# Kernel optimization log

Hardware: AMD Instinct MI355X
Metric: run time of the kernel (lower is better)

## Reference

```python
import jax, jax.numpy as jnp
import numpy as np

LRELU = 0.01  # torch nn.LeakyReLU default slope

def _lrelu(x):
    return jnp.where(x >= 0, x, LRELU * x)

def setup_inputs() -> dict:
    key = jax.random.key(0)
    ks = jax.random.split(key, 10)
    B, Cin, Cout, H, W, K, FD, LAT = 16, 256, 256, 64, 64, 3, 128, 128
    y = jax.random.normal(ks[0], (B, Cin, H, W), jnp.float32)
    finger = jax.random.randint(ks[1], (B, FD), 0, 2).astype(jnp.float32)
    ori_weight = jax.random.normal(ks[2], (Cout, Cin, K, K), jnp.float32) * 0.05
    w_mask = jax.random.normal(ks[3], (Cout, Cin, 1, 1), jnp.float32)
    f_weight = ori_weight[None]  # param initialized as 1*ori_weight, shape [1,Cout,Cin,K,K]
    style_w1 = jax.random.normal(ks[4], (LAT, FD), jnp.float32) / np.sqrt(FD)
    style_w2 = jax.random.normal(ks[5], (2 * Cin * K * K, LAT), jnp.float32) / np.sqrt(LAT)
    ori_bias = jax.random.normal(ks[6], (Cout,), jnp.float32) * 0.05
    b_mask = jax.random.normal(ks[7], (Cout,), jnp.float32)
    f_bias = ori_bias[None]  # [1,Cout]
    bias_w1 = jax.random.normal(ks[8], (Cout, FD), jnp.float32) / np.sqrt(FD)
    bias_w2 = jax.random.normal(ks[9], (Cout, Cout), jnp.float32) / np.sqrt(Cout)
    return dict(y=y, finger=finger, ori_weight=ori_weight, w_mask=w_mask,
                f_weight=f_weight, style_w1=style_w1, style_w2=style_w2,
                ori_bias=ori_bias, b_mask=b_mask, f_bias=f_bias,
                bias_w1=bias_w1, bias_w2=bias_w2)

def reference(y, finger, ori_weight, w_mask, f_weight, style_w1, style_w2,
              ori_bias, b_mask, f_bias, bias_w1, bias_w2):
    B = y.shape[0]
    Cout, Cin, K, _ = ori_weight.shape
    relu6 = lambda v: jnp.clip(v, 0.0, 6.0)
    # mask blending coefficients (w_mask broadcasts over the KxK taps, as in .repeat)
    f_w_weight = (6.0 - relu6(w_mask)) / 6.0          # [Cout,Cin,1,1]
    f_w_bias = (6.0 - relu6(b_mask)) / 6.0            # [Cout]
    mean_ori = ori_weight.mean()
    std_ori = jnp.std(ori_weight, ddof=1)             # torch .std() is unbiased
    # ApplyStyle: finger -> LAT -> 2*Cin*K*K scale/shift applied to f_weight
    h = _lrelu(finger @ style_w1.T)                   # [B,LAT]
    style = (h @ style_w2.T).reshape(B, 2, 1, Cin, K, K)
    s_weight = f_weight * (style[:, 0] + 1.0) + style[:, 1]  # [B,Cout,Cin,K,K]
    fw = f_w_weight[None]
    w1 = (1.0 - fw) * ori_weight[None] + fw * s_weight
    # per-sample whole-tensor re-standardization to ori stats
    mean = w1.mean(axis=(1, 2, 3, 4), keepdims=True)
    std = jnp.std(w1, axis=(1, 2, 3, 4), keepdims=True, ddof=1)
    w2 = (w1 - mean) / std * std_ori + mean_ori
    new_weight = (1.0 - fw) * ori_weight[None] + fw * w2      # [B,Cout,Cin,K,K]
    # per-sample bias
    s_bias = f_bias * _lrelu(_lrelu(finger @ bias_w1.T) @ bias_w2.T)  # [B,Cout]
    new_bias = (1.0 - f_w_bias) * ori_bias + f_w_bias * s_bias        # [B,Cout]
    pad = K // 2
    def conv_one(xi, wi, bi):
        o = jax.lax.conv_general_dilated(xi[None], wi, (1, 1),
                                         [(pad, pad), (pad, pad)],
                                         dimension_numbers=('NCHW', 'OIHW', 'NCHW'))
        return o[0] + bi[:, None, None]
    return jax.vmap(conv_one)(y, new_weight, new_bias)   # [B,Cout,H,W]
```

## Files before the change

kernel.cpp:

```cpp
#include <hip/hip_runtime.h>
#include <math.h>

#define LSLOPE 0.01f

__device__ __forceinline__ float lrelu(float x){ return x >= 0.f ? x : LSLOPE * x; }

typedef __attribute__((ext_vector_type(8))) short short8;
typedef __attribute__((ext_vector_type(4))) float f32x4;

__device__ __forceinline__ unsigned short f2bf(float f){
  union { float f; unsigned u; } v; v.f = f;
  unsigned r = v.u + 0x7FFFu + ((v.u >> 16) & 1u);
  return (unsigned short)(r >> 16);
}

__device__ __forceinline__ void gload_lds16(const unsigned short* g, unsigned short* l){
  __builtin_amdgcn_global_load_lds((const __attribute__((address_space(1))) unsigned int*)(g),
                                   (__attribute__((address_space(3))) unsigned int*)(l), 16, 0, 0);
}

constexpr int B    = 16;
constexpr int CIN  = 256;
constexpr int COUT = 256;
constexpr int HH   = 64;
constexpr int WW   = 64;
constexpr int FD   = 128;
constexpr int LAT  = 128;
constexpr int WPS  = CIN * 9;
constexpr int WTOT = COUT * WPS;
constexpr int HP   = 66;

constexpr int OFF_STAT  = 0;
constexpr int OFF_BMEAN = 16;
constexpr int OFF_BSTD  = 32;
constexpr int OFF_C     = 64;
constexpr int OFF_STYLE = OFF_C + 11 * WPS;
constexpr int OFF_NBIAS = OFF_STYLE + B * 2 * WPS;
constexpr int OFF_NW    = OFF_NBIAS + B * COUT;
constexpr int OFF_YTR   = OFF_NW + (B * 9 * COUT * CIN) / 2;

constexpr int PADT = 264;
constexpr int NB_CF = 9;
constexpr int NB_SB = B * 18 + B;
constexpr int NB_YT = HP * B;

__global__ __launch_bounds__(256) void k_prep1(const float* __restrict__ y, unsigned short* __restrict__ ytrp,
                                               const float* __restrict__ ow, const float* __restrict__ fwgt,
                                               const float* __restrict__ wmask, float* __restrict__ C,
                                               const float* __restrict__ finger, const float* __restrict__ sw1,
                                               const float* __restrict__ sw2, float* __restrict__ style,
                                               const float* __restrict__ bw1, const float* __restrict__ bw2,
                                               const float* __restrict__ fbias, const float* __restrict__ bmask,
                                               const float* __restrict__ obias, float* __restrict__ nbias){
  __shared__ __align__(16) char shraw[64 * PADT * 2];
  const int blk = blockIdx.x;
  const int tid = threadIdx.x;

  if (blk < NB_CF){
    const int rem = blk * 256 + tid;
    const int ic = rem / 9;
    float a_ow = 0.f, q_ow = 0.f, ab = 0.f, qb = 0.f;
    float a1 = 0.f, a2 = 0.f, d1 = 0.f, d2 = 0.f, d3 = 0.f, d4 = 0.f, d5 = 0.f;
    for (int oc = 0; oc < COUT; ++oc){
      float w = ow[(size_t)oc * WPS + rem];
      float f = fwgt[(size_t)oc * WPS + rem];
      float m = wmask[oc * CIN + ic];
      float fw = (6.f - fminf(fmaxf(m, 0.f), 6.f)) * (1.f / 6.f);
      float base = w + fw * (f - w);
      float c1 = fw * f, c2 = fw;
      a_ow += w; q_ow += w * w;
      ab += base; qb += base * base;
      a1 += c1; a2 += c2;
      d1 += c1 * c1; d2 += c2 * c2; d3 += base * c1; d4 += base * c2; d5 += c1 * c2;
    }
    C[(size_t)0  * WPS + rem] = a_ow; C[(size_t)1  * WPS + rem] = q_ow;
    C[(size_t)2  * WPS + rem] = ab;   C[(size_t)3  * WPS + rem] = qb;
    C[(size_t)4  * WPS + rem] = a1;   C[(size_t)5  * WPS + rem] = a2;
    C[(size_t)6  * WPS + rem] = d1;   C[(size_t)7  * WPS + rem] = d2;
    C[(size_t)8  * WPS + rem] = d3;   C[(size_t)9  * WPS + rem] = d4;
    C[(size_t)10 * WPS + rem] = d5;
  } else if (blk < NB_CF + NB_SB){
    float* sh = (float*)shraw;
    const int blk2 = blk - NB_CF;
    if (blk2 < B * 18){
      const int b = blk2 / 18, j0 = (blk2 - b * 18) * 256;
      if (tid < LAT){
        float a = 0.f;
        const float* fg = finger + b * FD;
        const float* w = sw1 + (size_t)tid * FD;
        for (int f = 0; f < FD; ++f) a += fg[f] * w[f];
        sh[tid] = lrelu(a);
      }
      __syncthreads();
      const int j = j0 + tid;
      float a = 0.f;
      const float* w2 = sw2 + (size_t)j * LAT;
      for (int l = 0; l < LAT; ++l) a += sh[l] * w2[l];
      style[(size_t)b * 2 * WPS + j] = a;
    } else {
      const int b = blk2 - B * 18, o = tid;
      float acc = 0.f;
      for (int f = 0; f < FD; ++f) acc += finger[b * FD + f] * bw1[o * FD + f];
      sh[o] = lrelu(acc);
      __syncthreads();
      float t = 0.f;
      for (int c = 0; c < COUT; ++c) t += sh[c] * bw2[o * COUT + c];
      t = lrelu(t);
      float sb = fbias[o] * t;
      float fwb = (6.f - fminf(fmaxf(bmask[o], 0.f), 6.f)) * (1.f / 6.f);
      nbias[b * COUT + o] = (1.f - fwb) * obias[o] + fwb * sb;
    }
  } else {
    unsigned short* t = (unsigned short*)shraw;
    const int blk3 = blk - NB_CF - NB_SB;
    const int ghp = blk3 % HP, b = blk3 / HP;
    unsigned short* dst = ytrp + ((size_t)b * HP + ghp) * HP * CIN;
    if (ghp == 0 || ghp == HP - 1){
      for (int c = tid; c < HP * CIN / 8; c += 256) ((uint4*)dst)[c] = (uint4){0, 0, 0, 0};
      return;
    }
    const int h = ghp - 1;
    const float* src = y + (size_t)b * CIN * HH * WW + h * WW;
    #pragma unroll
    for (int k = 0; k < 16; ++k){
      int idx = tid + k * 256;
      int ic = idx >> 4, w4 = (idx & 15) * 4;
      float4 v = *(const float4*)(src + (size_t)ic * HH * WW + w4);
      t[(w4 + 0) * PADT + ic] = f2bf(v.x);
      t[(w4 + 1) * PADT + ic] = f2bf(v.y);
      t[(w4 + 2) * PADT + ic] = f2bf(v.z);
      t[(w4 + 3) * PADT + ic] = f2bf(v.w);
    }
    __syncthreads();
    for (int c = tid; c < HP * CIN / 8; c += 256){
      int gwp = c >> 5, icg = (c & 31) * 8;
      uint4 v = (uint4){0, 0, 0, 0};
      if (gwp >= 1 && gwp <= 64) v = *(const uint4*)(&t[(gwp - 1) * PADT + icg]);
      ((uint4*)dst)[c] = v;
    }
  }
}

__global__ __launch_bounds__(256) void k_wstats(const float* __restrict__ C, const float* __restrict__ style,
                                                float* stat, float* bmean, float* bstd){
  __shared__ float rs[4][4];
  const int b = blockIdx.x, tid = threadIdx.x;
  const int lane = tid & 63, wid = tid >> 6;
  const float* st = style + (size_t)b * 2 * WPS;
  float s = 0.f, q = 0.f, so = 0.f, qo = 0.f;
  for (int k = 0; k < 9; ++k){
    int rem = k * 256 + tid;
    float aow = C[0 * WPS + rem], qow = C[1 * WPS + rem];
    float ab  = C[2 * WPS + rem], qb  = C[3 * WPS + rem];
    float a1  = C[4 * WPS + rem], a2  = C[5 * WPS + rem];
    float d1  = C[6 * WPS + rem], d2  = C[7 * WPS + rem];
    float d3  = C[8 * WPS + rem], d4  = C[9 * WPS + rem], d5 = C[10 * WPS + rem];
    float s0 = st[rem], s1 = st[WPS + rem];
    so += aow; qo += qow;
    s += ab + s0 * a1 + s1 * a2;
    q += qb + s0 * s0 * d1 + s1 * s1 * d2 + 2.f * (s0 * d3 + s1 * d4 + s0 * s1 * d5);
  }
  for (int o = 32; o > 0; o >>= 1){
    s += __shfl_down(s, o); q += __shfl_down(q, o);
    so += __shfl_down(so, o); qo += __shfl_down(qo, o);
  }
  if (lane == 0){ rs[0][wid] = s; rs[1][wid] = q; rs[2][wid] = so; rs[3][wid] = qo; }
  __syncthreads();
  if (tid == 0){
    const float N = (float)WTOT;
    float S = rs[0][0] + rs[0][1] + rs[0][2] + rs[0][3];
    float Q = rs[1][0] + rs[1][1] + rs[1][2] + rs[1][3];
    bmean[b] = S / N;
    bstd[b]  = sqrtf((Q - S * S / N) / (N - 1.f));
    if (b == 0){
      float SO = rs[2][0] + rs[2][1] + rs[2][2] + rs[2][3];
      float QO = rs[3][0] + rs[3][1] + rs[3][2] + rs[3][3];
      stat[0] = SO / N;
      stat[1] = sqrtf((QO - SO * SO / N) / (N - 1.f));
    }
  }
}

__global__ __launch_bounds__(256) void k_new_weight4(const float* __restrict__ ow, const float* __restrict__ fwgt,
                                                     const float* __restrict__ wmask, const float* __restrict__ style,
                                                     const float* __restrict__ stat, const float* __restrict__ bmean,
                                                     const float* __restrict__ bstd, unsigned short* __restrict__ nw){
  __shared__ float ows[WPS];
  __shared__ float fws[WPS];
  __shared__ float sts[2 * WPS];
  const int bi = blockIdx.x, oc = blockIdx.y;
  const int tid = threadIdx.x;
  const float mean_ori = stat[0], std_ori = stat[1];
  const float* owr = ow + (size_t)oc * WPS;
  const float* fwr = fwgt + (size_t)oc * WPS;
  for (int i = tid; i < WPS; i += 256){ ows[i] = owr[i]; fws[i] = fwr[i]; }
  const float fw = (6.f - fminf(fmaxf(wmask[oc * CIN + tid], 0.f), 6.f)) * (1.f / 6.f);
  #pragma unroll
  for (int bb = 0; bb < 2; ++bb){
    const int b = bi * 2 + bb;
    __syncthreads();
    const float* st = style + (size_t)b * 2 * WPS;
    for (int i = tid; i < 2 * WPS; i += 256) sts[i] = st[i];
    __syncthreads();
    const float bm = bmean[b], bs = bstd[b];
    #pragma unroll
    for (int t = 0; t < 9; ++t){
      int rem = tid * 9 + t;
      float owv = ows[rem];
      float sw = fws[rem] * (sts[rem] + 1.f) + sts[WPS + rem];
      float w1 = owv + fw * (sw - owv);
      float w2 = (w1 - bm) / bs * std_ori + mean_ori;
      nw[((size_t)(b * 9 + t) * COUT + oc) * CIN + tid] = f2bf(owv + fw * (w2 - owv));
    }
  }
}

__global__ __launch_bounds__(256, 2) void k_conv_mfma11(const unsigned short* __restrict__ ytrp,
                                                        const unsigned short* __restrict__ nw,
                                                        const float* __restrict__ nbias,
                                                        float* __restrict__ out){
  __shared__ __align__(16) unsigned short Wa[3 * 128 * 32];
  __shared__ __align__(16) unsigned short Yt[288 * 32];
  __shared__ float bsh[128];

  const int bid = blockIdx.x;
  const int xcd = bid & 7;
  const int b   = ((bid >> 8) << 3) | xcd;
  const int oc0 = ((bid >> 3) & 1) * 128;
  const int hwt = (bid >> 4) & 15;
  const int tid = threadIdx.x;
  const int lane = tid & 63, wid = tid >> 6;
  const int wr = wid >> 1, wc = wid & 1;
  const int hw0 = hwt * 256;
  const int h0  = hwt * 4;

  if (tid < 128) bsh[tid] = nbias[b * COUT + oc0 + tid];

  f32x4 acc[4][8];
  #pragma unroll
  for (int i = 0; i < 4; ++i)
    #pragma unroll
    for (int j = 0; j < 8; ++j) acc[i][j] = (f32x4){0.f, 0.f, 0.f, 0.f};

  const unsigned short* nwb = nw + ((size_t)(b * 9) * COUT + oc0) * CIN;
  const unsigned short* ytb = ytrp + (size_t)b * HP * HP * CIN;

  int a_tap[6], a_go[6], a_lo[6];
  #pragma unroll
  for (int s = 0; s < 6; ++s){
    int I = wid + 4 * s;
    int tap = I >> 3, rowbase = (I & 7) * 16;
    int row = rowbase + (lane >> 2), p = lane & 3;
    int g = p ^ ((row >> 1) & 3);
    a_tap[s] = tap;
    a_go[s]  = row * CIN + g * 8;
    a_lo[s]  = (tap * 128 + rowbase) * 32;
  }
  int y_go[5], y_lo[5]; bool y_has[5];
  #pragma unroll
  for (int s = 0; s < 5; ++s){
    int I = wid + 4 * s;
    y_has[s] = (I < 18);
    int Ic = y_has[s] ? I : 0;
    int site = Ic * 16 + (lane >> 2);
    int srow = site / 72;
    int scol = site - srow * 72;
    int gwp  = scol > 65 ? 65 : scol;
    int p = lane & 3, g = p ^ ((site >> 1) & 3);
    y_go[s] = ((h0 + srow + 1) * HP + gwp) * CIN + g * 8;
    y_lo[s] = Ic * 16 * 32;
  }

  const int gq = lane >> 4;
  int a_rb[4];
  #pragma unroll
  for (int mi = 0; mi < 4; ++mi){
    int r = wr * 64 + mi * 16 + (lane & 15);
    a_rb[mi] = r * 64 + ((gq ^ ((r >> 1) & 3)) << 4);
  }
  int b_site[8];
  #pragma unroll
  for (int ni = 0; ni < 8; ++ni)
    b_site[ni] = (wc * 2 + (ni >> 2)) * 72 + (ni & 3) * 16 + (lane & 15);

  #define STAGE(IT)                                                                 \
    {                                                                               \
      const int dhb = (IT) >> 3;                                                    \
      const int ic0s = ((IT) & 7) * 32;                                             \
      const unsigned short* ybase = ytb + (ptrdiff_t)(dhb - 1) * HP * CIN + ic0s;   \
      _Pragma("unroll")                                                             \
      for (int s = 0; s < 5; ++s)                                                   \
        if (y_has[s]) gload_lds16(ybase + y_go[s], &Yt[0] + y_lo[s]);               \
      const unsigned short* atap = nwb + (size_t)(dhb * 3) * COUT * CIN + ic0s;     \
      _Pragma("unroll")                                                             \
      for (int s = 0; s < 6; ++s)                                                   \
        gload_lds16(atap + (size_t)a_tap[s] * COUT * CIN + a_go[s], &Wa[0] + a_lo[s]); \
    }

  #define COMPUTE()                                                                 \
    {                                                                               \
      const char* wap = (const char*)&Wa[0];                                        \
      const char* ytp = (const char*)&Yt[0];                                        \
      _Pragma("unroll")                                                             \
      for (int tap = 0; tap < 3; ++tap){                                            \
        short8 af[4];                                                               \
        _Pragma("unroll")                                                           \
        for (int mi = 0; mi < 4; ++mi)                                              \
          af[mi] = *(const short8*)(wap + tap * 8192 + a_rb[mi]);                   \
        _Pragma("unroll")                                                           \
        for (int ni = 0; ni < 8; ++ni){                                             \
          const int site = b_site[ni] + tap;                                        \
          const int boff = (site << 6) + ((gq ^ ((site >> 1) & 3)) << 4);           \
          const short8 bf = *(const short8*)(ytp + boff);                           \
          _Pragma("unroll")                                                         \
          for (int mi = 0; mi < 4; ++mi)                                            \
            acc[mi][ni] = __builtin_amdgcn_mfma_f32_16x16x32_bf16(af[mi], bf, acc[mi][ni], 0, 0, 0); \
        }                                                                           \
      }                                                                             \
    }

  #pragma unroll 1
  for (int it = 0; it < 24; ++it){
    __syncthreads();
    STAGE(it);
    __syncthreads();
    COMPUTE();
  }
  #undef STAGE
  #undef COMPUTE

  const int col_l = lane & 15, row_l = (lane >> 4) * 4;
  #pragma unroll
  for (int mi = 0; mi < 4; ++mi){
    #pragma unroll
    for (int r = 0; r < 4; ++r){
      const int ocl = wr * 64 + mi * 16 + row_l + r;
      const float bb = bsh[ocl];
      float* op = out + ((size_t)(b * COUT + oc0 + ocl)) * (HH * WW) + hw0 + wc * 128;
      #pragma unroll
      for (int ni = 0; ni < 8; ++ni)
        op[(ni >> 2) * 64 + (ni & 3) * 16 + col_l] = acc[mi][ni][r] + bb;
    }
  }
}

extern "C" void kernel_launch(void* const* d_in, const int* in_sizes, int n_in,
                              void* d_out, int out_size, void* d_ws, size_t ws_size,
                              hipStream_t stream){
  const float* y      = (const float*)d_in[0];
  const float* finger = (const float*)d_in[1];
  const float* ow     = (const float*)d_in[2];
  const float* wmask  = (const float*)d_in[3];
  const float* fwgt   = (const float*)d_in[4];
  const float* sw1    = (const float*)d_in[5];
  const float* sw2    = (const float*)d_in[6];
  const float* obias  = (const float*)d_in[7];
  const float* bmask  = (const float*)d_in[8];
  const float* fbias  = (const float*)d_in[9];
  const float* bw1    = (const float*)d_in[10];
  const float* bw2    = (const float*)d_in[11];
  float* out = (float*)d_out;
  float* ws  = (float*)d_ws;

  float* stat  = ws + OFF_STAT;
  float* bmean = ws + OFF_BMEAN;
  float* bstd  = ws + OFF_BSTD;
  float* C     = ws + OFF_C;
  float* style = ws + OFF_STYLE;
  float* nbias = ws + OFF_NBIAS;
  unsigned short* nw   = (unsigned short*)(ws + OFF_NW);
  unsigned short* ytrp = (unsigned short*)(ws + OFF_YTR);

  k_prep1<<<NB_CF + NB_SB + NB_YT, 256, 0, stream>>>(y, ytrp, ow, fwgt, wmask, C,
                                                     finger, sw1, sw2, style,
                                                     bw1, bw2, fbias, bmask, obias, nbias);
  k_wstats<<<B, 256, 0, stream>>>(C, style, stat, bmean, bstd);
  k_new_weight4<<<dim3(B / 2, COUT), 256, 0, stream>>>(ow, fwgt, wmask, style, stat, bmean, bstd, nw);
  k_conv_mfma11<<<512, 256, 0, stream>>>(ytrp, nw, nbias, out);
}
```

Baseline: 139.9 us.

## Fuse weight stats into new-weight kernel and double-buffer conv with smaller tiles

```diff
diff --git a/kernel.cpp b/kernel.cpp
--- a/kernel.cpp
+++ b/kernel.cpp
@@ -30,9 +30,6 @@
 constexpr int WTOT = COUT * WPS;
 constexpr int HP   = 66;
 
-constexpr int OFF_STAT  = 0;
-constexpr int OFF_BMEAN = 16;
-constexpr int OFF_BSTD  = 32;
 constexpr int OFF_C     = 64;
 constexpr int OFF_STYLE = OFF_C + 11 * WPS;
 constexpr int OFF_NBIAS = OFF_STYLE + B * 2 * WPS;
@@ -141,68 +138,72 @@
   }
 }
 
-__global__ __launch_bounds__(256) void k_wstats(const float* __restrict__ C, const float* __restrict__ style,
-                                                float* stat, float* bmean, float* bstd){
-  __shared__ float rs[4][4];
-  const int b = blockIdx.x, tid = threadIdx.x;
-  const int lane = tid & 63, wid = tid >> 6;
-  const float* st = style + (size_t)b * 2 * WPS;
-  float s = 0.f, q = 0.f, so = 0.f, qo = 0.f;
-  for (int k = 0; k < 9; ++k){
-    int rem = k * 256 + tid;
-    float aow = C[0 * WPS + rem], qow = C[1 * WPS + rem];
-    float ab  = C[2 * WPS + rem], qb  = C[3 * WPS + rem];
-    float a1  = C[4 * WPS + rem], a2  = C[5 * WPS + rem];
-    float d1  = C[6 * WPS + rem], d2  = C[7 * WPS + rem];
-    float d3  = C[8 * WPS + rem], d4  = C[9 * WPS + rem], d5 = C[10 * WPS + rem];
-    float s0 = st[rem], s1 = st[WPS + rem];
-    so += aow; qo += qow;
-    s += ab + s0 * a1 + s1 * a2;
-    q += qb + s0 * s0 * d1 + s1 * s1 * d2 + 2.f * (s0 * d3 + s1 * d4 + s0 * s1 * d5);
-  }
-  for (int o = 32; o > 0; o >>= 1){
-    s += __shfl_down(s, o); q += __shfl_down(q, o);
-    so += __shfl_down(so, o); qo += __shfl_down(qo, o);
-  }
-  if (lane == 0){ rs[0][wid] = s; rs[1][wid] = q; rs[2][wid] = so; rs[3][wid] = qo; }
-  __syncthreads();
-  if (tid == 0){
-    const float N = (float)WTOT;
-    float S = rs[0][0] + rs[0][1] + rs[0][2] + rs[0][3];
-    float Q = rs[1][0] + rs[1][1] + rs[1][2] + rs[1][3];
-    bmean[b] = S / N;
-    bstd[b]  = sqrtf((Q - S * S / N) / (N - 1.f));
-    if (b == 0){
-      float SO = rs[2][0] + rs[2][1] + rs[2][2] + rs[2][3];
-      float QO = rs[3][0] + rs[3][1] + rs[3][2] + rs[3][3];
-      stat[0] = SO / N;
-      stat[1] = sqrtf((QO - SO * SO / N) / (N - 1.f));
-    }
-  }
-}
-
-__global__ __launch_bounds__(256) void k_new_weight4(const float* __restrict__ ow, const float* __restrict__ fwgt,
+__global__ __launch_bounds__(256) void k_new_weight5(const float* __restrict__ ow, const float* __restrict__ fwgt,
                                                      const float* __restrict__ wmask, const float* __restrict__ style,
-                                                     const float* __restrict__ stat, const float* __restrict__ bmean,
-                                                     const float* __restrict__ bstd, unsigned short* __restrict__ nw){
+                                                     const float* __restrict__ C, unsigned short* __restrict__ nw){
   __shared__ float ows[WPS];
   __shared__ float fws[WPS];
   __shared__ float sts[2 * WPS];
+  __shared__ float red[2][4];
+  __shared__ float bcast[4];
   const int bi = blockIdx.x, oc = blockIdx.y;
   const int tid = threadIdx.x;
-  const float mean_ori = stat[0], std_ori = stat[1];
+  const int lane = tid & 63, wid = tid >> 6;
   const float* owr = ow + (size_t)oc * WPS;
   const float* fwr = fwgt + (size_t)oc * WPS;
   for (int i = tid; i < WPS; i += 256){ ows[i] = owr[i]; fws[i] = fwr[i]; }
   const float fw = (6.f - fminf(fmaxf(wmask[oc * CIN + tid], 0.f), 6.f)) * (1.f / 6.f);
-  #pragma unroll
-  for (int bb = 0; bb < 2; ++bb){
-    const int b = bi * 2 + bb;
+
+  {
+    float so = 0.f, qo = 0.f;
+    for (int k = 0; k < 9; ++k){
+      int rem = k * 256 + tid;
+      so += C[0 * WPS + rem]; qo += C[1 * WPS + rem];
+    }
+    for (int o = 32; o > 0; o >>= 1){ so += __shfl_down(so, o); qo += __shfl_down(qo, o); }
+    if (lane == 0){ red[0][wid] = so; red[1][wid] = qo; }
+    __syncthreads();
+    if (tid == 0){
+      const float N = (float)WTOT;
+      float SO = red[0][0] + red[0][1] + red[0][2] + red[0][3];
+      float QO = red[1][0] + red[1][1] + red[1][2] + red[1][3];
+      bcast[2] = SO / N;
+      bcast[3] = sqrtf((QO - SO * SO / N) / (N - 1.f));
+    }
+    __syncthreads();
+  }
+  const float mean_ori = bcast[2], std_ori = bcast[3];
+
+  #pragma unroll 1
+  for (int bb = 0; bb < 4; ++bb){
+    const int b = bi * 4 + bb;
     __syncthreads();
     const float* st = style + (size_t)b * 2 * WPS;
     for (int i = tid; i < 2 * WPS; i += 256) sts[i] = st[i];
     __syncthreads();
-    const float bm = bmean[b], bs = bstd[b];
+    float s = 0.f, q = 0.f;
+    for (int k = 0; k < 9; ++k){
+      int rem = k * 256 + tid;
+      float ab = C[2 * WPS + rem], qb = C[3 * WPS + rem];
+      float a1 = C[4 * WPS + rem], a2 = C[5 * WPS + rem];
+      float d1 = C[6 * WPS + rem], d2 = C[7 * WPS + rem];
+      float d3 = C[8 * WPS + rem], d4 = C[9 * WPS + rem], d5 = C[10 * WPS + rem];
+      float s0 = sts[rem], s1 = sts[WPS + rem];
+      s += ab + s0 * a1 + s1 * a2;
+      q += qb + s0 * s0 * d1 + s1 * s1 * d2 + 2.f * (s0 * d3 + s1 * d4 + s0 * s1 * d5);
+    }
+    for (int o = 32; o > 0; o >>= 1){ s += __shfl_down(s, o); q += __shfl_down(q, o); }
+    if (lane == 0){ red[0][wid] = s; red[1][wid] = q; }
+    __syncthreads();
+    if (tid == 0){
+      const float N = (float)WTOT;
+      float S = red[0][0] + red[0][1] + red[0][2] + red[0][3];
+      float Q = red[1][0] + red[1][1] + red[1][2] + red[1][3];
+      bcast[0] = S / N;
+      bcast[1] = sqrtf((Q - S * S / N) / (N - 1.f));
+    }
+    __syncthreads();
+    const float bm = bcast[0], bs = bcast[1];
     #pragma unroll
     for (int t = 0; t < 9; ++t){
       int rem = tid * 9 + t;
@@ -215,32 +216,35 @@
   }
 }
 
-__global__ __launch_bounds__(256, 2) void k_conv_mfma11(const unsigned short* __restrict__ ytrp,
+__global__ __launch_bounds__(256, 2) void k_conv_mfma13(const unsigned short* __restrict__ ytrp,
                                                         const unsigned short* __restrict__ nw,
                                                         const float* __restrict__ nbias,
                                                         float* __restrict__ out){
-  __shared__ __align__(16) unsigned short Wa[3 * 128 * 32];
-  __shared__ __align__(16) unsigned short Yt[288 * 32];
+  constexpr int WASTRIDE = 3 * 128 * 32;
+  constexpr int YTSTRIDE = 144 * 32;
+  __shared__ __align__(16) unsigned short Wa[2 * WASTRIDE];
+  __shared__ __align__(16) unsigned short Yt[2 * YTSTRIDE];
   __shared__ float bsh[128];
 
   const int bid = blockIdx.x;
-  const int xcd = bid & 7;
-  const int b   = ((bid >> 8) << 3) | xcd;
-  const int oc0 = ((bid >> 3) & 1) * 128;
-  const int hwt = (bid >> 4) & 15;
+  const int xcd = bid & 7, idx = bid >> 3;
+  const int b   = ((idx >> 6) << 3) | xcd;
+  const int rem6 = idx & 63;
+  const int oc0 = (rem6 & 1) * 128;
+  const int hwt = rem6 >> 1;
   const int tid = threadIdx.x;
   const int lane = tid & 63, wid = tid >> 6;
   const int wr = wid >> 1, wc = wid & 1;
-  const int hw0 = hwt * 256;
-  const int h0  = hwt * 4;
+  const int hw0 = hwt * 128;
+  const int h0  = hwt * 2;
 
   if (tid < 128) bsh[tid] = nbias[b * COUT + oc0 + tid];
 
-  f32x4 acc[4][8];
+  f32x4 acc[4][4];
   #pragma unroll
   for (int i = 0; i < 4; ++i)
     #pragma unroll
-    for (int j = 0; j < 8; ++j) acc[i][j] = (f32x4){0.f, 0.f, 0.f, 0.f};
+    for (int j = 0; j < 4; ++j) acc[i][j] = (f32x4){0.f, 0.f, 0.f, 0.f};
 
   const unsigned short* nwb = nw + ((size_t)(b * 9) * COUT + oc0) * CIN;
   const unsigned short* ytb = ytrp + (size_t)b * HP * HP * CIN;
@@ -256,14 +260,14 @@
     a_go[s]  = row * CIN + g * 8;
     a_lo[s]  = (tap * 128 + rowbase) * 32;
   }
-  int y_go[5], y_lo[5]; bool y_has[5];
-  #pragma unroll
-  for (int s = 0; s < 5; ++s){
+  int y_go[3], y_lo[3]; bool y_has[3];
+  #pragma unroll
+  for (int s = 0; s < 3; ++s){
     int I = wid + 4 * s;
-    y_has[s] = (I < 18);
+    y_has[s] = (I < 9);
     int Ic = y_has[s] ? I : 0;
     int site = Ic * 16 + (lane >> 2);
-    int srow = site / 72;
+    int srow = (site >= 72) ? 1 : 0;
     int scol = site - srow * 72;
     int gwp  = scol > 65 ? 65 : scol;
     int p = lane & 3, g = p ^ ((site >> 1) & 3);
@@ -278,29 +282,31 @@
     int r = wr * 64 + mi * 16 + (lane & 15);
     a_rb[mi] = r * 64 + ((gq ^ ((r >> 1) & 3)) << 4);
   }
-  int b_site[8];
-  #pragma unroll
-  for (int ni = 0; ni < 8; ++ni)
-    b_site[ni] = (wc * 2 + (ni >> 2)) * 72 + (ni & 3) * 16 + (lane & 15);
-
-  #define STAGE(IT)                                                                 \
+  int b_site[4];
+  #pragma unroll
+  for (int ni = 0; ni < 4; ++ni)
+    b_site[ni] = wc * 72 + ni * 16 + (lane & 15);
+
+  #define STAGE(BUF, IT)                                                            \
     {                                                                               \
       const int dhb = (IT) >> 3;                                                    \
       const int ic0s = ((IT) & 7) * 32;                                             \
+      unsigned short* wb = &Wa[(BUF) * WASTRIDE];                                   \
+      unsigned short* yb = &Yt[(BUF) * YTSTRIDE];                                   \
       const unsigned short* ybase = ytb + (ptrdiff_t)(dhb - 1) * HP * CIN + ic0s;   \
       _Pragma("unroll")                                                             \
-      for (int s = 0; s < 5; ++s)                                                   \
-        if (y_has[s]) gload_lds16(ybase + y_go[s], &Yt[0] + y_lo[s]);               \
+      for (int s = 0; s < 3; ++s)                                                   \
+        if (y_has[s]) gload_lds16(ybase + y_go[s], yb + y_lo[s]);                   \
       const unsigned short* atap = nwb + (size_t)(dhb * 3) * COUT * CIN + ic0s;     \
       _Pragma("unroll")                                                             \
       for (int s = 0; s < 6; ++s)                                                   \
-        gload_lds16(atap + (size_t)a_tap[s] * COUT * CIN + a_go[s], &Wa[0] + a_lo[s]); \
-    }
-
-  #define COMPUTE()                                                                 \
+        gload_lds16(atap + (size_t)a_tap[s] * COUT * CIN + a_go[s], wb + a_lo[s]);  \
+    }
+
+  #define COMPUTE(BUF)                                                              \
     {                                                                               \
-      const char* wap = (const char*)&Wa[0];                                        \
-      const char* ytp = (const char*)&Yt[0];                                        \
+      const char* wap = (const char*)&Wa[(BUF) * WASTRIDE];                         \
+      const char* ytp = (const char*)&Yt[(BUF) * YTSTRIDE];                         \
       _Pragma("unroll")                                                             \
       for (int tap = 0; tap < 3; ++tap){                                            \
         short8 af[4];                                                               \
@@ -308,7 +314,7 @@
         for (int mi = 0; mi < 4; ++mi)                                              \
           af[mi] = *(const short8*)(wap + tap * 8192 + a_rb[mi]);                   \
         _Pragma("unroll")                                                           \
-        for (int ni = 0; ni < 8; ++ni){                                             \
+        for (int ni = 0; ni < 4; ++ni){                                             \
           const int site = b_site[ni] + tap;                                        \
           const int boff = (site << 6) + ((gq ^ ((site >> 1) & 3)) << 4);           \
           const short8 bf = *(const short8*)(ytp + boff);                           \
@@ -319,12 +325,16 @@
       }                                                                             \
     }
 
+  STAGE(0, 0);
+  STAGE(1, 1);
   #pragma unroll 1
   for (int it = 0; it < 24; ++it){
-    __syncthreads();
-    STAGE(it);
-    __syncthreads();
-    COMPUTE();
+    if (it < 23) asm volatile("s_waitcnt vmcnt(8)" ::: "memory");
+    else         asm volatile("s_waitcnt vmcnt(0)" ::: "memory");
+    asm volatile("s_barrier" ::: "memory");
+    COMPUTE(it & 1);
+    asm volatile("s_barrier" ::: "memory");
+    if (it + 2 < 24){ STAGE(it & 1, it + 2); }
   }
   #undef STAGE
   #undef COMPUTE
@@ -336,10 +346,10 @@
     for (int r = 0; r < 4; ++r){
       const int ocl = wr * 64 + mi * 16 + row_l + r;
       const float bb = bsh[ocl];
-      float* op = out + ((size_t)(b * COUT + oc0 + ocl)) * (HH * WW) + hw0 + wc * 128;
+      float* op = out + ((size_t)(b * COUT + oc0 + ocl)) * (HH * WW) + hw0 + wc * 64;
       #pragma unroll
-      for (int ni = 0; ni < 8; ++ni)
-        op[(ni >> 2) * 64 + (ni & 3) * 16 + col_l] = acc[mi][ni][r] + bb;
+      for (int ni = 0; ni < 4; ++ni)
+        op[ni * 16 + col_l] = acc[mi][ni][r] + bb;
     }
   }
 }
@@ -362,9 +372,6 @@
   float* out = (float*)d_out;
   float* ws  = (float*)d_ws;
 
-  float* stat  = ws + OFF_STAT;
-  float* bmean = ws + OFF_BMEAN;
-  float* bstd  = ws + OFF_BSTD;
   float* C     = ws + OFF_C;
   float* style = ws + OFF_STYLE;
   float* nbias = ws + OFF_NBIAS;
@@ -374,7 +381,6 @@
   k_prep1<<<NB_CF + NB_SB + NB_YT, 256, 0, stream>>>(y, ytrp, ow, fwgt, wmask, C,
                                                      finger, sw1, sw2, style,
                                                      bw1, bw2, fbias, bmask, obias, nbias);
-  k_wstats<<<B, 256, 0, stream>>>(C, style, stat, bmean, bstd);
-  k_new_weight4<<<dim3(B / 2, COUT), 256, 0, stream>>>(ow, fwgt, wmask, style, stat, bmean, bstd, nw);
-  k_conv_mfma11<<<512, 256, 0, stream>>>(ytrp, nw, nbias, out);
-}
+  k_new_weight5<<<dim3(4, COUT), 256, 0, stream>>>(ow, fwgt, wmask, style, C, nw);
+  k_conv_mfma13<<<1024, 256, 0, stream>>>(ytrp, nw, nbias, out);
+}
```

After: 144.9 us. 1.04x slower.
